# Performance work log

Hardware: AMD Instinct MI355X
Metric: run time of the kernel (lower is better)

## Reference

```python
import jax, jax.numpy as jnp
import numpy as np

B, K, D, NL = 16, 2048, 512, 2
DI = 2 * D  # expand=2


def _ln(x, w, b, eps=1e-5):
    m = x.mean(-1, keepdims=True)
    v = ((x - m) ** 2).mean(-1, keepdims=True)
    return (x - m) / jnp.sqrt(v + eps) * w + b


def setup_inputs() -> dict:
    key = jax.random.key(0)
    ks = iter(jax.random.split(key, 64))
    w = lambda shape: jax.random.normal(next(ks), shape, jnp.float32) * 0.02
    d = {
        's': jax.random.normal(next(ks), (B, K, D), jnp.float32),
        'km': jnp.ones((B, K), jnp.float32),
    }
    for p in ('fwd', 'bwd'):
        d[p + '_ln_w'] = jnp.ones((NL, D), jnp.float32)
        d[p + '_ln_b'] = jnp.zeros((NL, D), jnp.float32)
        d[p + '_pin_w'] = w((NL, 2 * DI, D))
        d[p + '_pin_b'] = jnp.zeros((NL, 2 * DI), jnp.float32)
        d[p + '_pout_w'] = w((NL, D, DI))
        d[p + '_pout_b'] = jnp.zeros((NL, D), jnp.float32)
        d[p + '_iln_w'] = jnp.ones((NL, DI), jnp.float32)
        d[p + '_iln_b'] = jnp.zeros((NL, DI), jnp.float32)
    d['mrg_w'] = w((NL, D, 2 * D))
    d['mrg_b'] = jnp.zeros((NL, D), jnp.float32)
    d['nrm_w'] = jnp.ones((NL, D), jnp.float32)
    d['nrm_b'] = jnp.zeros((NL, D), jnp.float32)
    d['ffn_ln_w'] = jnp.ones((NL, D), jnp.float32)
    d['ffn_ln_b'] = jnp.zeros((NL, D), jnp.float32)
    d['ffn_w1'] = w((NL, 4 * D, D))
    d['ffn_b1'] = jnp.zeros((NL, 4 * D), jnp.float32)
    d['ffn_w2'] = w((NL, D, 4 * D))
    d['ffn_b2'] = jnp.zeros((NL, D), jnp.float32)
    return d


def _ssm(x, lnw, lnb, pinw, pinb, poutw, poutb, ilnw, ilnb):
    # SSMBlock (LinearAttention fallback path): x + proj_out(LN(silu(z)*sigmoid(g)))
    h = _ln(x, lnw, lnb)
    zg = h @ pinw.T + pinb          # [B,K,2*DI]
    z, g = jnp.split(zg, 2, axis=-1)
    y = _ln(jax.nn.silu(z) * jax.nn.sigmoid(g), ilnw, ilnb)
    return x + y @ poutw.T + poutb


def _forward(s, km,
             fwd_ln_w, fwd_ln_b, fwd_pin_w, fwd_pin_b, fwd_pout_w, fwd_pout_b, fwd_iln_w, fwd_iln_b,
             bwd_ln_w, bwd_ln_b, bwd_pin_w, bwd_pin_b, bwd_pout_w, bwd_pout_b, bwd_iln_w, bwd_iln_b,
             mrg_w, mrg_b, nrm_w, nrm_b,
             ffn_ln_w, ffn_ln_b, ffn_w1, ffn_b1, ffn_w2, ffn_b2):
    for i in range(NL):
        r = s
        # sort nodes by descending L2 norm (per batch row)
        o = jnp.argsort(-jnp.linalg.norm(s, axis=-1), axis=-1)  # [B,K]
        so = jnp.take_along_axis(s, o[..., None], axis=1)        # gather
        f = _ssm(so, fwd_ln_w[i], fwd_ln_b[i], fwd_pin_w[i], fwd_pin_b[i],
                 fwd_pout_w[i], fwd_pout_b[i], fwd_iln_w[i], fwd_iln_b[i])
        b = jnp.flip(_ssm(jnp.flip(so, 1), bwd_ln_w[i], bwd_ln_b[i], bwd_pin_w[i], bwd_pin_b[i],
                          bwd_pout_w[i], bwd_pout_b[i], bwd_iln_w[i], bwd_iln_b[i]), 1)
        rv = jnp.argsort(o, axis=-1)                             # inverse permutation
        m = jnp.concatenate([f, b], axis=-1) @ mrg_w[i].T + mrg_b[i]
        s = _ln(r + jnp.take_along_axis(m, rv[..., None], axis=1), nrm_w[i], nrm_b[i])
        h = _ln(s, ffn_ln_w[i], ffn_ln_b[i])
        h = jax.nn.gelu(h @ ffn_w1[i].T + ffn_b1[i], approximate=False)
        s = s + h @ ffn_w2[i].T + ffn_b2[i]
        s = s * km[..., None]
    return s


def reference(s, km,
              fwd_ln_w, fwd_ln_b, fwd_pin_w, fwd_pin_b, fwd_pout_w, fwd_pout_b, fwd_iln_w, fwd_iln_b,
              bwd_ln_w, bwd_ln_b, bwd_pin_w, bwd_pin_b, bwd_pout_w, bwd_pout_b, bwd_iln_w, bwd_iln_b,
              mrg_w, mrg_b, nrm_w, nrm_b,
              ffn_ln_w, ffn_ln_b, ffn_w1, ffn_b1, ffn_w2, ffn_b2):
    return _forward(s, km,
                    fwd_ln_w, fwd_ln_b, fwd_pin_w, fwd_pin_b, fwd_pout_w, fwd_pout_b, fwd_iln_w, fwd_iln_b,
                    bwd_ln_w, bwd_ln_b, bwd_pin_w, bwd_pin_b, bwd_pout_w, bwd_pout_b, bwd_iln_w, bwd_iln_b,
                    mrg_w, mrg_b, nrm_w, nrm_b,
                    ffn_ln_w, ffn_ln_b, ffn_w1, ffn_b1, ffn_w2, ffn_b2)
```

## Files before the change

kernel.cpp:

```cpp
#include <hip/hip_runtime.h>
#include <math.h>

typedef unsigned short u16;
typedef __attribute__((ext_vector_type(8))) short short8;
typedef __attribute__((ext_vector_type(4))) float f32x4;
typedef __attribute__((ext_vector_type(4))) unsigned short u16x4;

#define DEV static __device__ __forceinline__

DEV float b2f(u16 u) { unsigned v = ((unsigned)u) << 16; float f; __builtin_memcpy(&f, &v, 4); return f; }
DEV u16 f2b(float f) {
  unsigned u; __builtin_memcpy(&u, &f, 4);
  u += 0x7fffu + ((u >> 16) & 1u);
  return (u16)(u >> 16);
}

DEV float wred(float v) {
#pragma unroll
  for (int m = 1; m < 64; m <<= 1) v += __shfl_xor(v, m, 64);
  return v;
}

DEV void gld_lds16(const u16* src, u16* lds_dst) {
  __builtin_amdgcn_global_load_lds(
      (const __attribute__((address_space(1))) void*)src,
      (__attribute__((address_space(3))) void*)lds_dst, 16, 0, 0);
}

template <int EPI>
__global__ __launch_bounds__(256, 2) void gemm_tn(
    const u16* __restrict__ A, const u16* __restrict__ W, const int K,
    const float* __restrict__ bias, const float* __restrict__ res,
    const float* __restrict__ kmask, float* __restrict__ outF,
    u16* __restrict__ outB, const int coloff) {
  __shared__ u16 Ash[2][128 * 64];
  __shared__ u16 Bsh[2][128 * 64];
  const int tid = threadIdx.x;
  const int wid = tid >> 6;
  const int lane = tid & 63;
  const int bn = blockIdx.x;
  const int m0 = blockIdx.y << 7;

  f32x4 acc[2][8];
#pragma unroll
  for (int a = 0; a < 2; ++a)
#pragma unroll
    for (int b = 0; b < 8; ++b) acc[a][b] = f32x4{0.f, 0.f, 0.f, 0.f};

  auto stage = [&](int buf, int k0) {
#pragma unroll
    for (int c = 0; c < 4; ++c) {
      const int j = wid * 256 + c * 64 + lane;
      const int row = j >> 3, cc = j & 7;
      const int scc = cc ^ (row & 7);
      const u16* src = A + (size_t)(m0 + row) * K + k0 + scc * 8;
      gld_lds16(src, &Ash[buf][(wid * 256 + c * 64) * 8]);
    }
#pragma unroll
    for (int c = 0; c < 4; ++c) {
      const int j = wid * 256 + c * 64 + lane;
      const int row = j >> 3, cc = j & 7;
      const int scc = cc ^ (row & 7);
      int wrow;
      if constexpr (EPI == 0)
        wrow = (row < 64) ? (bn * 64 + row) : (1024 + bn * 64 + (row - 64));
      else
        wrow = bn * 128 + row;
      const u16* src = W + (size_t)wrow * K + k0 + scc * 8;
      gld_lds16(src, &Bsh[buf][(wid * 256 + c * 64) * 8]);
    }
  };

  stage(0, 0);
  const int KT = K >> 6;
  for (int kt = 0; kt < KT; ++kt) {
    const int cur = kt & 1;
    __syncthreads();
    if (kt + 1 < KT) stage(cur ^ 1, (kt + 1) << 6);
    const char* Ab = (const char*)(&Ash[cur][0]);
    const char* Bb = (const char*)(&Bsh[cur][0]);
#pragma unroll
    for (int kk = 0; kk < 2; ++kk) {
      const int cbb = kk * 64 + ((lane >> 4) << 4);
      short8 af[2];
#pragma unroll
      for (int mf = 0; mf < 2; ++mf) {
        const int row = wid * 32 + mf * 16 + (lane & 15);
        af[mf] = *(const short8*)(Ab + row * 128 + (cbb ^ ((row & 7) << 4)));
      }
      short8 bfr[8];
#pragma unroll
      for (int cf = 0; cf < 8; ++cf) {
        const int row = cf * 16 + (lane & 15);
        bfr[cf] = *(const short8*)(Bb + row * 128 + (cbb ^ ((row & 7) << 4)));
      }
#pragma unroll
      for (int mf = 0; mf < 2; ++mf)
#pragma unroll
        for (int cf = 0; cf < 8; ++cf)
          acc[mf][cf] = __builtin_amdgcn_mfma_f32_16x16x32_bf16(af[mf], bfr[cf], acc[mf][cf], 0, 0, 0);
    }
  }

  const int lc = lane & 15;
  const int lr = (lane >> 4) << 2;
  const int gm0 = m0 + wid * 32;

  if constexpr (EPI == 0) {
#pragma unroll
    for (int mf = 0; mf < 2; ++mf)
#pragma unroll
      for (int cf = 0; cf < 4; ++cf) {
        const int col = bn * 64 + cf * 16 + lc;
        const float bz = bias[col];
        const float bg = bias[1024 + col];
#pragma unroll
        for (int r = 0; r < 4; ++r) {
          const int m = gm0 + mf * 16 + lr + r;
          const float z = acc[mf][cf][r] + bz;
          const float g = acc[mf][cf + 4][r] + bg;
          const float y = z / (1.f + __expf(-z)) * (1.f / (1.f + __expf(-g)));
          outB[(size_t)m * 1024 + col] = f2b(y);
        }
      }
  } else if constexpr (EPI == 1) {
#pragma unroll
    for (int mf = 0; mf < 2; ++mf)
#pragma unroll
      for (int cf = 0; cf < 8; ++cf) {
        const int col = bn * 128 + cf * 16 + lc;
        const float bv = bias[col];
#pragma unroll
        for (int r = 0; r < 4; ++r) {
          const int m = gm0 + mf * 16 + lr + r;
          const float v = acc[mf][cf][r] + bv + res[(size_t)m * 512 + col];
          outB[(size_t)m * 1024 + coloff + col] = f2b(v);
        }
      }
  } else if constexpr (EPI == 2) {
#pragma unroll
    for (int mf = 0; mf < 2; ++mf)
#pragma unroll
      for (int cf = 0; cf < 8; ++cf) {
        const int col = bn * 128 + cf * 16 + lc;
        const float bv = bias[col];
#pragma unroll
        for (int r = 0; r < 4; ++r) {
          const int m = gm0 + mf * 16 + lr + r;
          outF[(size_t)m * 512 + col] = acc[mf][cf][r] + bv + res[(size_t)m * 512 + col];
        }
      }
  } else if constexpr (EPI == 3) {
#pragma unroll
    for (int mf = 0; mf < 2; ++mf)
#pragma unroll
      for (int cf = 0; cf < 8; ++cf) {
        const int col = bn * 128 + cf * 16 + lc;
        const float bv = bias[col];
#pragma unroll
        for (int r = 0; r < 4; ++r) {
          const int m = gm0 + mf * 16 + lr + r;
          const float v = acc[mf][cf][r] + bv;
          outB[(size_t)m * 2048 + col] = f2b(0.5f * v * (1.f + erff(v * 0.70710678f)));
        }
      }
  } else {
#pragma unroll
    for (int mf = 0; mf < 2; ++mf)
#pragma unroll
      for (int cf = 0; cf < 8; ++cf) {
        const int col = bn * 128 + cf * 16 + lc;
        const float bv = bias[col];
#pragma unroll
        for (int r = 0; r < 4; ++r) {
          const int m = gm0 + mf * 16 + lr + r;
          outF[(size_t)m * 512 + col] =
              (acc[mf][cf][r] + bv + res[(size_t)m * 512 + col]) * kmask[m];
        }
      }
  }
}

__global__ void dual_ln_512(const float* __restrict__ x,
                            const float* __restrict__ w1, const float* __restrict__ b1,
                            const float* __restrict__ w2, const float* __restrict__ b2,
                            u16* __restrict__ o1, u16* __restrict__ o2) {
  const int row = blockIdx.x * 4 + (threadIdx.x >> 6);
  const int lane = threadIdx.x & 63;
  const float* xr = x + (size_t)row * 512;
  float v[8];
  *(float4*)&v[0] = *(const float4*)(xr + lane * 4);
  *(float4*)&v[4] = *(const float4*)(xr + 256 + lane * 4);
  float s = 0.f, q = 0.f;
#pragma unroll
  for (int j = 0; j < 8; ++j) { s += v[j]; q += v[j] * v[j]; }
  s = wred(s); q = wred(q);
  const float mean = s * (1.f / 512.f);
  const float rstd = rsqrtf(q * (1.f / 512.f) - mean * mean + 1e-5f);
  float wa[8], ba[8], wb[8], bb[8];
  *(float4*)&wa[0] = *(const float4*)(w1 + lane * 4);
  *(float4*)&wa[4] = *(const float4*)(w1 + 256 + lane * 4);
  *(float4*)&ba[0] = *(const float4*)(b1 + lane * 4);
  *(float4*)&ba[4] = *(const float4*)(b1 + 256 + lane * 4);
  *(float4*)&wb[0] = *(const float4*)(w2 + lane * 4);
  *(float4*)&wb[4] = *(const float4*)(w2 + 256 + lane * 4);
  *(float4*)&bb[0] = *(const float4*)(b2 + lane * 4);
  *(float4*)&bb[4] = *(const float4*)(b2 + 256 + lane * 4);
  u16 oa[8], ob[8];
#pragma unroll
  for (int j = 0; j < 8; ++j) {
    const float nv = (v[j] - mean) * rstd;
    oa[j] = f2b(nv * wa[j] + ba[j]);
    ob[j] = f2b(nv * wb[j] + bb[j]);
  }
  *(u16x4*)(o1 + (size_t)row * 512 + lane * 4) = *(u16x4*)&oa[0];
  *(u16x4*)(o1 + (size_t)row * 512 + 256 + lane * 4) = *(u16x4*)&oa[4];
  *(u16x4*)(o2 + (size_t)row * 512 + lane * 4) = *(u16x4*)&ob[0];
  *(u16x4*)(o2 + (size_t)row * 512 + 256 + lane * 4) = *(u16x4*)&ob[4];
}

__global__ void ln_bf16_1024(u16* __restrict__ y, const float* __restrict__ w,
                             const float* __restrict__ b) {
  const int row = blockIdx.x * 4 + (threadIdx.x >> 6);
  const int lane = threadIdx.x & 63;
  u16* yr = y + (size_t)row * 1024;
  const short8 a0 = *(const short8*)(yr + lane * 8);
  const short8 a1 = *(const short8*)(yr + 512 + lane * 8);
  float v[16];
#pragma unroll
  for (int j = 0; j < 8; ++j) { v[j] = b2f((u16)a0[j]); v[8 + j] = b2f((u16)a1[j]); }
  float s = 0.f, q = 0.f;
#pragma unroll
  for (int j = 0; j < 16; ++j) { s += v[j]; q += v[j] * v[j]; }
  s = wred(s); q = wred(q);
  const float mean = s * (1.f / 1024.f);
  const float rstd = rsqrtf(q * (1.f / 1024.f) - mean * mean + 1e-5f);
  float wv[16], bv[16];
  *(float4*)&wv[0] = *(const float4*)(w + lane * 8);
  *(float4*)&wv[4] = *(const float4*)(w + lane * 8 + 4);
  *(float4*)&wv[8] = *(const float4*)(w + 512 + lane * 8);
  *(float4*)&wv[12] = *(const float4*)(w + 512 + lane * 8 + 4);
  *(float4*)&bv[0] = *(const float4*)(b + lane * 8);
  *(float4*)&bv[4] = *(const float4*)(b + lane * 8 + 4);
  *(float4*)&bv[8] = *(const float4*)(b + 512 + lane * 8);
  *(float4*)&bv[12] = *(const float4*)(b + 512 + lane * 8 + 4);
  u16 o[16];
#pragma unroll
  for (int j = 0; j < 16; ++j) o[j] = f2b((v[j] - mean) * rstd * wv[j] + bv[j]);
  *(short8*)(yr + lane * 8) = *(short8*)&o[0];
  *(short8*)(yr + 512 + lane * 8) = *(short8*)&o[8];
}

__global__ void dual_ln_t(float* __restrict__ t,
                          const float* __restrict__ nw, const float* __restrict__ nb,
                          const float* __restrict__ fw, const float* __restrict__ fb,
                          u16* __restrict__ h) {
  const int row = blockIdx.x * 4 + (threadIdx.x >> 6);
  const int lane = threadIdx.x & 63;
  float* tr = t + (size_t)row * 512;
  float v[8];
  *(float4*)&v[0] = *(const float4*)(tr + lane * 4);
  *(float4*)&v[4] = *(const float4*)(tr + 256 + lane * 4);
  float s = 0.f, q = 0.f;
#pragma unroll
  for (int j = 0; j < 8; ++j) { s += v[j]; q += v[j] * v[j]; }
  s = wred(s); q = wred(q);
  const float mean = s * (1.f / 512.f);
  const float rstd = rsqrtf(q * (1.f / 512.f) - mean * mean + 1e-5f);
  float nwv[8], nbv[8], fwv[8], fbv[8];
  *(float4*)&nwv[0] = *(const float4*)(nw + lane * 4);
  *(float4*)&nwv[4] = *(const float4*)(nw + 256 + lane * 4);
  *(float4*)&nbv[0] = *(const float4*)(nb + lane * 4);
  *(float4*)&nbv[4] = *(const float4*)(nb + 256 + lane * 4);
  *(float4*)&fwv[0] = *(const float4*)(fw + lane * 4);
  *(float4*)&fwv[4] = *(const float4*)(fw + 256 + lane * 4);
  *(float4*)&fbv[0] = *(const float4*)(fb + lane * 4);
  *(float4*)&fbv[4] = *(const float4*)(fb + 256 + lane * 4);
  float tv[8];
#pragma unroll
  for (int j = 0; j < 8; ++j) tv[j] = (v[j] - mean) * rstd * nwv[j] + nbv[j];
  *(float4*)(tr + lane * 4) = *(float4*)&tv[0];
  *(float4*)(tr + 256 + lane * 4) = *(float4*)&tv[4];
  float s2 = 0.f, q2 = 0.f;
#pragma unroll
  for (int j = 0; j < 8; ++j) { s2 += tv[j]; q2 += tv[j] * tv[j]; }
  s2 = wred(s2); q2 = wred(q2);
  const float mean2 = s2 * (1.f / 512.f);
  const float rstd2 = rsqrtf(q2 * (1.f / 512.f) - mean2 * mean2 + 1e-5f);
  u16 o[8];
#pragma unroll
  for (int j = 0; j < 8; ++j) o[j] = f2b((tv[j] - mean2) * rstd2 * fwv[j] + fbv[j]);
  *(u16x4*)(h + (size_t)row * 512 + lane * 4) = *(u16x4*)&o[0];
  *(u16x4*)(h + (size_t)row * 512 + 256 + lane * 4) = *(u16x4*)&o[4];
}

__global__ void cvt_f32_bf16(const float* __restrict__ s, u16* __restrict__ d, const int n) {
  const int i = (blockIdx.x * 256 + threadIdx.x) * 4;
  if (i >= n) return;
  const float4 v = *(const float4*)(s + i);
  u16x4 o = {f2b(v.x), f2b(v.y), f2b(v.z), f2b(v.w)};
  *(u16x4*)(d + i) = o;
}

extern "C" void kernel_launch(void* const* d_in, const int* in_sizes, int n_in,
                              void* d_out, int out_size, void* d_ws, size_t ws_size,
                              hipStream_t stream) {
  (void)in_sizes; (void)n_in; (void)out_size; (void)ws_size;
  constexpr int M = 16 * 2048;

  const float* s0        = (const float*)d_in[0];
  const float* km        = (const float*)d_in[1];
  const float* fwd_ln_w  = (const float*)d_in[2];
  const float* fwd_ln_b  = (const float*)d_in[3];
  const float* fwd_pin_w = (const float*)d_in[4];
  const float* fwd_pin_b = (const float*)d_in[5];
  const float* fwd_pout_w= (const float*)d_in[6];
  const float* fwd_pout_b= (const float*)d_in[7];
  const float* fwd_iln_w = (const float*)d_in[8];
  const float* fwd_iln_b = (const float*)d_in[9];
  const float* bwd_ln_w  = (const float*)d_in[10];
  const float* bwd_ln_b  = (const float*)d_in[11];
  const float* bwd_pin_w = (const float*)d_in[12];
  const float* bwd_pin_b = (const float*)d_in[13];
  const float* bwd_pout_w= (const float*)d_in[14];
  const float* bwd_pout_b= (const float*)d_in[15];
  const float* bwd_iln_w = (const float*)d_in[16];
  const float* bwd_iln_b = (const float*)d_in[17];
  const float* mrg_w     = (const float*)d_in[18];
  const float* mrg_b     = (const float*)d_in[19];
  const float* nrm_w     = (const float*)d_in[20];
  const float* nrm_b     = (const float*)d_in[21];
  const float* ffn_ln_w  = (const float*)d_in[22];
  const float* ffn_ln_b  = (const float*)d_in[23];
  const float* ffn_w1    = (const float*)d_in[24];
  const float* ffn_b1    = (const float*)d_in[25];
  const float* ffn_w2    = (const float*)d_in[26];
  const float* ffn_b2    = (const float*)d_in[27];

  char* p = (char*)d_ws;
  auto alloc = [&](size_t bytes) { char* r = p; p += bytes; return r; };
  float* T  = (float*)alloc((size_t)M * 512 * 4);
  u16* Xf   = (u16*)alloc((size_t)M * 512 * 2);
  u16* YH   = (u16*)alloc((size_t)M * 2048 * 2);
  u16* Wss  = (u16*)alloc((size_t)2048 * 512 * 2);
  u16* Xb = (u16*)T;
  u16* Y  = YH;
  u16* FB = YH + (size_t)M * 1024;
  u16* H1 = YH;

  for (int L = 0; L < 2; ++L) {
    const float* sin = L ? (const float*)d_out : s0;
    float* sout = (float*)d_out;
    dual_ln_512<<<M / 4, 256, 0, stream>>>(sin, fwd_ln_w + L * 512, fwd_ln_b + L * 512,
                                           bwd_ln_w + L * 512, bwd_ln_b + L * 512, Xf, Xb);
    cvt_f32_bf16<<<1024, 256, 0, stream>>>(fwd_pin_w + (size_t)L * 2048 * 512, Wss, 2048 * 512);
    gemm_tn<0><<<dim3(16, M / 128), 256, 0, stream>>>(Xf, Wss, 512,
        fwd_pin_b + L * 2048, nullptr, nullptr, nullptr, Y, 0);
    ln_bf16_1024<<<M / 4, 256, 0, stream>>>(Y, fwd_iln_w + L * 1024, fwd_iln_b + L * 1024);
    cvt_f32_bf16<<<512, 256, 0, stream>>>(fwd_pout_w + (size_t)L * 512 * 1024, Wss, 512 * 1024);
    gemm_tn<1><<<dim3(4, M / 128), 256, 0, stream>>>(Y, Wss, 1024,
        fwd_pout_b + L * 512, sin, nullptr, nullptr, FB, 0);
    cvt_f32_bf16<<<1024, 256, 0, stream>>>(bwd_pin_w + (size_t)L * 2048 * 512, Wss, 2048 * 512);
    gemm_tn<0><<<dim3(16, M / 128), 256, 0, stream>>>(Xb, Wss, 512,
        bwd_pin_b + L * 2048, nullptr, nullptr, nullptr, Y, 0);
    ln_bf16_1024<<<M / 4, 256, 0, stream>>>(Y, bwd_iln_w + L * 1024, bwd_iln_b + L * 1024);
    cvt_f32_bf16<<<512, 256, 0, stream>>>(bwd_pout_w + (size_t)L * 512 * 1024, Wss, 512 * 1024);
    gemm_tn<1><<<dim3(4, M / 128), 256, 0, stream>>>(Y, Wss, 1024,
        bwd_pout_b + L * 512, sin, nullptr, nullptr, FB, 512);
    cvt_f32_bf16<<<512, 256, 0, stream>>>(mrg_w + (size_t)L * 512 * 1024, Wss, 512 * 1024);
    gemm_tn<2><<<dim3(4, M / 128), 256, 0, stream>>>(FB, Wss, 1024,
        mrg_b + L * 512, sin, nullptr, T, nullptr, 0);
    dual_ln_t<<<M / 4, 256, 0, stream>>>(T, nrm_w + L * 512, nrm_b + L * 512,
                                         ffn_ln_w + L * 512, ffn_ln_b + L * 512, Xf);
    cvt_f32_bf16<<<1024, 256, 0, stream>>>(ffn_w1 + (size_t)L * 2048 * 512, Wss, 2048 * 512);
    gemm_tn<3><<<dim3(16, M / 128), 256, 0, stream>>>(Xf, Wss, 512,
        ffn_b1 + L * 2048, nullptr, nullptr, nullptr, H1, 0);
    cvt_f32_bf16<<<1024, 256, 0, stream>>>(ffn_w2 + (size_t)L * 512 * 2048, Wss, 512 * 2048);
    gemm_tn<4><<<dim3(4, M / 128), 256, 0, stream>>>(H1, Wss, 2048,
        ffn_b2 + L * 512, T, km, sout, nullptr, 0);
  }
}
```

Measured before the change: 1.602 ms.

## Replace GEMM with 128x256 tile, 8-wave, triple-buffered LDS pipeline

```diff
diff --git a/kernel.cpp b/kernel.cpp
--- a/kernel.cpp
+++ b/kernel.cpp
@@ -28,154 +28,170 @@
 }
 
 template <int EPI>
-__global__ __launch_bounds__(256, 2) void gemm_tn(
-    const u16* __restrict__ A, const u16* __restrict__ W, const int K,
+__global__ __launch_bounds__(512, 1) void gemm_big(
+    const u16* __restrict__ A, const int lda, const u16* __restrict__ W, const int K,
     const float* __restrict__ bias, const float* __restrict__ res,
     const float* __restrict__ kmask, float* __restrict__ outF,
     u16* __restrict__ outB, const int coloff) {
-  __shared__ u16 Ash[2][128 * 64];
-  __shared__ u16 Bsh[2][128 * 64];
+  __shared__ u16 sh[3 * 24576];
   const int tid = threadIdx.x;
   const int wid = tid >> 6;
   const int lane = tid & 63;
+  const int wr = wid >> 2;
+  const int wc = wid & 3;
   const int bn = blockIdx.x;
   const int m0 = blockIdx.y << 7;
 
-  f32x4 acc[2][8];
-#pragma unroll
-  for (int a = 0; a < 2; ++a)
-#pragma unroll
-    for (int b = 0; b < 8; ++b) acc[a][b] = f32x4{0.f, 0.f, 0.f, 0.f};
-
-  auto stage = [&](int buf, int k0) {
-#pragma unroll
-    for (int c = 0; c < 4; ++c) {
-      const int j = wid * 256 + c * 64 + lane;
-      const int row = j >> 3, cc = j & 7;
-      const int scc = cc ^ (row & 7);
-      const u16* src = A + (size_t)(m0 + row) * K + k0 + scc * 8;
-      gld_lds16(src, &Ash[buf][(wid * 256 + c * 64) * 8]);
+  f32x4 acc[4][4];
+#pragma unroll
+  for (int a = 0; a < 4; ++a)
+#pragma unroll
+    for (int b = 0; b < 4; ++b) acc[a][b] = f32x4{0.f, 0.f, 0.f, 0.f};
+
+  const int KT = K >> 6;
+
+  auto issue = [&](int kt) {
+    const int st = kt % 3;
+    const int k0 = kt << 6;
+#pragma unroll
+    for (int i = 0; i < 2; ++i) {
+      const int jb = wid * 1024 + i * 8192;
+      const int j = jb + lane * 16;
+      const int row = j >> 7, c = (j >> 4) & 7;
+      const u16* src = A + (size_t)(m0 + row) * lda + k0 + ((c ^ (row & 7)) << 3);
+      gld_lds16(src, &sh[st * 24576 + (jb >> 1)]);
     }
 #pragma unroll
-    for (int c = 0; c < 4; ++c) {
-      const int j = wid * 256 + c * 64 + lane;
-      const int row = j >> 3, cc = j & 7;
-      const int scc = cc ^ (row & 7);
+    for (int i = 0; i < 4; ++i) {
+      const int jb = wid * 1024 + i * 8192;
+      const int j = jb + lane * 16;
+      const int row = j >> 7, c = (j >> 4) & 7;
       int wrow;
-      if constexpr (EPI == 0)
-        wrow = (row < 64) ? (bn * 64 + row) : (1024 + bn * 64 + (row - 64));
-      else
-        wrow = bn * 128 + row;
-      const u16* src = W + (size_t)wrow * K + k0 + scc * 8;
-      gld_lds16(src, &Bsh[buf][(wid * 256 + c * 64) * 8]);
+      if constexpr (EPI == 0) {
+        const int s = row >> 6, t = row & 63;
+        wrow = (t < 32) ? (bn * 128 + s * 32 + t) : (1024 + bn * 128 + s * 32 + (t - 32));
+      } else {
+        wrow = bn * 256 + row;
+      }
+      const u16* src = W + (size_t)wrow * K + k0 + ((c ^ (row & 7)) << 3);
+      gld_lds16(src, &sh[st * 24576 + 8192 + (jb >> 1)]);
     }
   };
 
-  stage(0, 0);
-  const int KT = K >> 6;
+  issue(0);
+  issue(1);
+  asm volatile("s_waitcnt vmcnt(6)" ::: "memory");
+  __builtin_amdgcn_s_barrier();
+  __builtin_amdgcn_sched_barrier(0);
+
   for (int kt = 0; kt < KT; ++kt) {
-    const int cur = kt & 1;
-    __syncthreads();
-    if (kt + 1 < KT) stage(cur ^ 1, (kt + 1) << 6);
-    const char* Ab = (const char*)(&Ash[cur][0]);
-    const char* Bb = (const char*)(&Bsh[cur][0]);
+    const char* Ab = (const char*)&sh[(kt % 3) * 24576];
+    const char* Bb = Ab + 16384;
+    if (kt + 2 < KT) issue(kt + 2);
 #pragma unroll
     for (int kk = 0; kk < 2; ++kk) {
       const int cbb = kk * 64 + ((lane >> 4) << 4);
-      short8 af[2];
-#pragma unroll
-      for (int mf = 0; mf < 2; ++mf) {
-        const int row = wid * 32 + mf * 16 + (lane & 15);
+      short8 af[4], bf[4];
+#pragma unroll
+      for (int mf = 0; mf < 4; ++mf) {
+        const int row = wr * 64 + mf * 16 + (lane & 15);
         af[mf] = *(const short8*)(Ab + row * 128 + (cbb ^ ((row & 7) << 4)));
       }
-      short8 bfr[8];
-#pragma unroll
-      for (int cf = 0; cf < 8; ++cf) {
-        const int row = cf * 16 + (lane & 15);
-        bfr[cf] = *(const short8*)(Bb + row * 128 + (cbb ^ ((row & 7) << 4)));
-      }
-#pragma unroll
-      for (int mf = 0; mf < 2; ++mf)
-#pragma unroll
-        for (int cf = 0; cf < 8; ++cf)
-          acc[mf][cf] = __builtin_amdgcn_mfma_f32_16x16x32_bf16(af[mf], bfr[cf], acc[mf][cf], 0, 0, 0);
+#pragma unroll
+      for (int nf = 0; nf < 4; ++nf) {
+        const int row = wc * 64 + nf * 16 + (lane & 15);
+        bf[nf] = *(const short8*)(Bb + row * 128 + (cbb ^ ((row & 7) << 4)));
+      }
+      __builtin_amdgcn_s_setprio(1);
+#pragma unroll
+      for (int mf = 0; mf < 4; ++mf)
+#pragma unroll
+        for (int nf = 0; nf < 4; ++nf)
+          acc[mf][nf] = __builtin_amdgcn_mfma_f32_16x16x32_bf16(af[mf], bf[nf], acc[mf][nf], 0, 0, 0);
+      __builtin_amdgcn_s_setprio(0);
+    }
+    if (kt + 1 < KT) {
+      if (kt + 2 < KT) asm volatile("s_waitcnt vmcnt(6)" ::: "memory");
+      else             asm volatile("s_waitcnt vmcnt(0)" ::: "memory");
+      __builtin_amdgcn_s_barrier();
+      __builtin_amdgcn_sched_barrier(0);
     }
   }
 
   const int lc = lane & 15;
   const int lr = (lane >> 4) << 2;
-  const int gm0 = m0 + wid * 32;
+  const int gm0 = m0 + wr * 64;
 
   if constexpr (EPI == 0) {
 #pragma unroll
-    for (int mf = 0; mf < 2; ++mf)
-#pragma unroll
-      for (int cf = 0; cf < 4; ++cf) {
-        const int col = bn * 64 + cf * 16 + lc;
+    for (int mf = 0; mf < 4; ++mf)
+#pragma unroll
+      for (int nf = 0; nf < 2; ++nf) {
+        const int col = bn * 128 + wc * 32 + nf * 16 + lc;
         const float bz = bias[col];
         const float bg = bias[1024 + col];
 #pragma unroll
         for (int r = 0; r < 4; ++r) {
           const int m = gm0 + mf * 16 + lr + r;
-          const float z = acc[mf][cf][r] + bz;
-          const float g = acc[mf][cf + 4][r] + bg;
+          const float z = acc[mf][nf][r] + bz;
+          const float g = acc[mf][nf + 2][r] + bg;
           const float y = z / (1.f + __expf(-z)) * (1.f / (1.f + __expf(-g)));
           outB[(size_t)m * 1024 + col] = f2b(y);
         }
       }
   } else if constexpr (EPI == 1) {
 #pragma unroll
-    for (int mf = 0; mf < 2; ++mf)
-#pragma unroll
-      for (int cf = 0; cf < 8; ++cf) {
-        const int col = bn * 128 + cf * 16 + lc;
+    for (int mf = 0; mf < 4; ++mf)
+#pragma unroll
+      for (int nf = 0; nf < 4; ++nf) {
+        const int col = bn * 256 + wc * 64 + nf * 16 + lc;
         const float bv = bias[col];
 #pragma unroll
         for (int r = 0; r < 4; ++r) {
           const int m = gm0 + mf * 16 + lr + r;
-          const float v = acc[mf][cf][r] + bv + res[(size_t)m * 512 + col];
+          const float v = acc[mf][nf][r] + bv + res[(size_t)m * 512 + col];
           outB[(size_t)m * 1024 + coloff + col] = f2b(v);
         }
       }
   } else if constexpr (EPI == 2) {
 #pragma unroll
-    for (int mf = 0; mf < 2; ++mf)
-#pragma unroll
-      for (int cf = 0; cf < 8; ++cf) {
-        const int col = bn * 128 + cf * 16 + lc;
+    for (int mf = 0; mf < 4; ++mf)
+#pragma unroll
+      for (int nf = 0; nf < 4; ++nf) {
+        const int col = bn * 256 + wc * 64 + nf * 16 + lc;
         const float bv = bias[col];
 #pragma unroll
         for (int r = 0; r < 4; ++r) {
           const int m = gm0 + mf * 16 + lr + r;
-          outF[(size_t)m * 512 + col] = acc[mf][cf][r] + bv + res[(size_t)m * 512 + col];
+          outF[(size_t)m * 512 + col] = acc[mf][nf][r] + bv + res[(size_t)m * 512 + col];
         }
       }
   } else if constexpr (EPI == 3) {
 #pragma unroll
-    for (int mf = 0; mf < 2; ++mf)
-#pragma unroll
-      for (int cf = 0; cf < 8; ++cf) {
-        const int col = bn * 128 + cf * 16 + lc;
+    for (int mf = 0; mf < 4; ++mf)
+#pragma unroll
+      for (int nf = 0; nf < 4; ++nf) {
+        const int col = bn * 256 + wc * 64 + nf * 16 + lc;
         const float bv = bias[col];
 #pragma unroll
         for (int r = 0; r < 4; ++r) {
           const int m = gm0 + mf * 16 + lr + r;
-          const float v = acc[mf][cf][r] + bv;
+          const float v = acc[mf][nf][r] + bv;
           outB[(size_t)m * 2048 + col] = f2b(0.5f * v * (1.f + erff(v * 0.70710678f)));
         }
       }
   } else {
 #pragma unroll
-    for (int mf = 0; mf < 2; ++mf)
-#pragma unroll
-      for (int cf = 0; cf < 8; ++cf) {
-        const int col = bn * 128 + cf * 16 + lc;
+    for (int mf = 0; mf < 4; ++mf)
+#pragma unroll
+      for (int nf = 0; nf < 4; ++nf) {
+        const int col = bn * 256 + wc * 64 + nf * 16 + lc;
         const float bv = bias[col];
 #pragma unroll
         for (int r = 0; r < 4; ++r) {
           const int m = gm0 + mf * 16 + lr + r;
           outF[(size_t)m * 512 + col] =
-              (acc[mf][cf][r] + bv + res[(size_t)m * 512 + col]) * kmask[m];
+              (acc[mf][nf][r] + bv + res[(size_t)m * 512 + col]) * kmask[m];
         }
       }
   }
@@ -341,42 +357,43 @@
   auto alloc = [&](size_t bytes) { char* r = p; p += bytes; return r; };
   float* T  = (float*)alloc((size_t)M * 512 * 4);
   u16* Xf   = (u16*)alloc((size_t)M * 512 * 2);
-  u16* YH   = (u16*)alloc((size_t)M * 2048 * 2);
+  u16* ZH   = (u16*)alloc((size_t)M * 2048 * 2);
   u16* Wss  = (u16*)alloc((size_t)2048 * 512 * 2);
   u16* Xb = (u16*)T;
-  u16* Y  = YH;
-  u16* FB = YH + (size_t)M * 1024;
-  u16* H1 = YH;
-
+  u16* Y  = ZH;
+  u16* FB = ZH + (size_t)M * 1024;
+  u16* H1 = ZH;
+
+  const dim3 blk(512);
   for (int L = 0; L < 2; ++L) {
     const float* sin = L ? (const float*)d_out : s0;
     float* sout = (float*)d_out;
     dual_ln_512<<<M / 4, 256, 0, stream>>>(sin, fwd_ln_w + L * 512, fwd_ln_b + L * 512,
                                            bwd_ln_w + L * 512, bwd_ln_b + L * 512, Xf, Xb);
     cvt_f32_bf16<<<1024, 256, 0, stream>>>(fwd_pin_w + (size_t)L * 2048 * 512, Wss, 2048 * 512);
-    gemm_tn<0><<<dim3(16, M / 128), 256, 0, stream>>>(Xf, Wss, 512,
+    gemm_big<0><<<dim3(8, M / 128), blk, 0, stream>>>(Xf, 512, Wss, 512,
         fwd_pin_b + L * 2048, nullptr, nullptr, nullptr, Y, 0);
     ln_bf16_1024<<<M / 4, 256, 0, stream>>>(Y, fwd_iln_w + L * 1024, fwd_iln_b + L * 1024);
     cvt_f32_bf16<<<512, 256, 0, stream>>>(fwd_pout_w + (size_t)L * 512 * 1024, Wss, 512 * 1024);
-    gemm_tn<1><<<dim3(4, M / 128), 256, 0, stream>>>(Y, Wss, 1024,
+    gemm_big<1><<<dim3(2, M / 128), blk, 0, stream>>>(Y, 1024, Wss, 1024,
         fwd_pout_b + L * 512, sin, nullptr, nullptr, FB, 0);
     cvt_f32_bf16<<<1024, 256, 0, stream>>>(bwd_pin_w + (size_t)L * 2048 * 512, Wss, 2048 * 512);
-    gemm_tn<0><<<dim3(16, M / 128), 256, 0, stream>>>(Xb, Wss, 512,
+    gemm_big<0><<<dim3(8, M / 128), blk, 0, stream>>>(Xb, 512, Wss, 512,
         bwd_pin_b + L * 2048, nullptr, nullptr, nullptr, Y, 0);
     ln_bf16_1024<<<M / 4, 256, 0, stream>>>(Y, bwd_iln_w + L * 1024, bwd_iln_b + L * 1024);
     cvt_f32_bf16<<<512, 256, 0, stream>>>(bwd_pout_w + (size_t)L * 512 * 1024, Wss, 512 * 1024);
-    gemm_tn<1><<<dim3(4, M / 128), 256, 0, stream>>>(Y, Wss, 1024,
+    gemm_big<1><<<dim3(2, M / 128), blk, 0, stream>>>(Y, 1024, Wss, 1024,
         bwd_pout_b + L * 512, sin, nullptr, nullptr, FB, 512);
     cvt_f32_bf16<<<512, 256, 0, stream>>>(mrg_w + (size_t)L * 512 * 1024, Wss, 512 * 1024);
-    gemm_tn<2><<<dim3(4, M / 128), 256, 0, stream>>>(FB, Wss, 1024,
+    gemm_big<2><<<dim3(2, M / 128), blk, 0, stream>>>(FB, 1024, Wss, 1024,
         mrg_b + L * 512, sin, nullptr, T, nullptr, 0);
     dual_ln_t<<<M / 4, 256, 0, stream>>>(T, nrm_w + L * 512, nrm_b + L * 512,
                                          ffn_ln_w + L * 512, ffn_ln_b + L * 512, Xf);
     cvt_f32_bf16<<<1024, 256, 0, stream>>>(ffn_w1 + (size_t)L * 2048 * 512, Wss, 2048 * 512);
-    gemm_tn<3><<<dim3(16, M / 128), 256, 0, stream>>>(Xf, Wss, 512,
+    gemm_big<3><<<dim3(8, M / 128), blk, 0, stream>>>(Xf, 512, Wss, 512,
         ffn_b1 + L * 2048, nullptr, nullptr, nullptr, H1, 0);
     cvt_f32_bf16<<<1024, 256, 0, stream>>>(ffn_w2 + (size_t)L * 512 * 2048, Wss, 512 * 2048);
-    gemm_tn<4><<<dim3(4, M / 128), 256, 0, stream>>>(H1, Wss, 2048,
+    gemm_big<4><<<dim3(2, M / 128), blk, 0, stream>>>(H1, 2048, Wss, 2048,
         ffn_b2 + L * 512, T, km, sout, nullptr, 0);
   }
 }
```

Result: faster. 1.555 ms (-2.9%).
